# Performance work log

Hardware: AMD Instinct MI355X
Metric: run time of the kernel (lower is better)

## Reference

```python
import jax, jax.numpy as jnp
import numpy as np


def setup_inputs() -> dict:
    key = jax.random.key(0)
    ks = jax.random.split(key, 7)
    B, S, D_IN, D_K, D_V = 4, 4096, 1024, 64, 64
    s = 1.0 / np.sqrt(D_IN)
    return {
        "query": jax.random.normal(ks[0], (B, S, D_IN), jnp.float32),
        "key": jax.random.normal(ks[1], (B, S, D_IN), jnp.float32),
        "value": jax.random.normal(ks[2], (B, S, D_IN), jnp.float32),
        "Wq": jax.random.normal(ks[3], (D_IN, D_K), jnp.float32) * s,
        "bq": jnp.zeros((D_K,), jnp.float32),
        "Wk": jax.random.normal(ks[4], (D_IN, D_K), jnp.float32) * s,
        "bk": jnp.zeros((D_K,), jnp.float32),
        "Wv": jax.random.normal(ks[5], (D_IN, D_V), jnp.float32) * s,
        "bv": jnp.zeros((D_V,), jnp.float32),
    }


def reference(query, key, value, Wq, bq, Wk, bk, Wv, bv):
    # q(query) is computed twice in the original but is identical; compute once.
    q = query @ Wq + bq            # [B,S,dk]
    k = key @ Wk + bk              # [B,S,dk]
    v = value @ Wv + bv            # [B,S,dv]
    scale = jnp.asarray(q.shape[-1] ** 0.5, q.dtype)
    scores = jnp.einsum("bqd,bkd->bqk", q, k) / scale  # [B,S,S]
    probs = jax.nn.softmax(scores, axis=-1)
    return jnp.einsum("bqk,bkd->bqd", probs, v)        # [B,S,dv]
```

## Files before the change

kernel.cpp:

```cpp
#include <hip/hip_runtime.h>
#include <cmath>

constexpr int B_  = 4;
constexpr int S_  = 4096;
constexpr int DIN = 1024;
constexpr int DH  = 64;

typedef short bf16x8 __attribute__((ext_vector_type(8)));
typedef float f32x4  __attribute__((ext_vector_type(4)));

#define GPTR(p) (const __attribute__((address_space(1))) unsigned int*)(p)
#define LPTR(p) (__attribute__((address_space(3))) unsigned int*)(p)

__device__ __forceinline__ ushort f2bf(float x) {
    unsigned int u = __float_as_uint(x);
    return (ushort)((u + 0x7FFFu + ((u >> 16) & 1u)) >> 16);
}

__device__ __forceinline__ bf16x8 cvt8(float4 a, float4 b) {
    union { bf16x8 v; ushort u[8]; } r;
    r.u[0] = f2bf(a.x); r.u[1] = f2bf(a.y); r.u[2] = f2bf(a.z); r.u[3] = f2bf(a.w);
    r.u[4] = f2bf(b.x); r.u[5] = f2bf(b.y); r.u[6] = f2bf(b.z); r.u[7] = f2bf(b.w);
    return r.v;
}

#define QSCALE 0.18033688011112042f

__global__ __launch_bounds__(256) void setup_w(
    const float* __restrict__ Wq, const float* __restrict__ Wk,
    const float* __restrict__ Wv, ushort* __restrict__ Wt_g)
{
    const int y = blockIdx.y;
    const float* W = (y == 0) ? Wq : (y == 1) ? Wk : Wv;
    const int g    = blockIdx.x * 256 + threadIdx.x;
    const int lane = g & 63;
    const int nt   = (g >> 6) & 3;
    const int ks   = (g >> 8) & 1;
    const int it   = g >> 9;
    const int m    = lane & 15;
    const int quad = lane >> 4;
    const int n    = nt * 16 + m;
    const int k0   = it * 64 + (ks * 4 + quad) * 8;
    union { uint4 q; ushort u[8]; } r;
    #pragma unroll
    for (int i = 0; i < 8; ++i) r.u[i] = f2bf(W[(size_t)(k0 + i) * DH + n]);
    *(uint4*)(Wt_g + ((size_t)y << 16) + (size_t)g * 8) = r.q;
}

__global__ __launch_bounds__(256, 3) void proj_kernel(
    const float* __restrict__ Xq, const float* __restrict__ Xk, const float* __restrict__ Xv,
    const float* __restrict__ bq, const float* __restrict__ bk, const float* __restrict__ bv,
    const ushort* __restrict__ Wt_g,
    ushort* __restrict__ Qb, ushort* __restrict__ Kb, ushort* __restrict__ Vt)
{
    const int y = blockIdx.y;
    const float *X, *bias;
    if (y == 0)      { X = Xq; bias = bq; }
    else if (y == 1) { X = Xk; bias = bk; }
    else             { X = Xv; bias = bv; }

    __shared__ ushort Vx[64 * 72];

    const int tid  = threadIdx.x;
    const int w    = tid >> 6;
    const int lane = tid & 63;
    const int m    = lane & 15;
    const int quad = lane >> 4;
    const int row0 = blockIdx.x * 64;
    const int ph0  = (blockIdx.x + blockIdx.y * 5) & 15;

    const size_t  xrow = (size_t)(row0 + w * 16 + m) * DIN;
    const ushort* wsrc = Wt_g + ((size_t)y << 16) + (size_t)lane * 8;

    float bias_v[4];
    #pragma unroll
    for (int nt = 0; nt < 4; ++nt) bias_v[nt] = bias[nt * 16 + m];

    f32x4 acc[4] = {};
    float4 xb[2][4];
    uint4  wb[2][8];

    {
        const float* px = X + xrow + ph0 * 64 + quad * 8;
        xb[0][0] = *(const float4*)(px);      xb[0][1] = *(const float4*)(px + 4);
        xb[0][2] = *(const float4*)(px + 32); xb[0][3] = *(const float4*)(px + 36);
        #pragma unroll
        for (int f = 0; f < 8; ++f)
            wb[0][f] = *(const uint4*)(wsrc + (size_t)(ph0 * 8 + f) * 512);
    }

    #pragma unroll
    for (int it = 0; it < 16; ++it) {
        const int cb = it & 1, nb = cb ^ 1;
        if (it < 15) {
            const int wi = (it + 1 + ph0) & 15;
            const float* px = X + xrow + wi * 64 + quad * 8;
            xb[nb][0] = *(const float4*)(px);      xb[nb][1] = *(const float4*)(px + 4);
            xb[nb][2] = *(const float4*)(px + 32); xb[nb][3] = *(const float4*)(px + 36);
            #pragma unroll
            for (int f = 0; f < 8; ++f)
                wb[nb][f] = *(const uint4*)(wsrc + (size_t)(wi * 8 + f) * 512);
        }
        __builtin_amdgcn_sched_barrier(0);
        #pragma unroll
        for (int ks = 0; ks < 2; ++ks) {
            const bf16x8 a = cvt8(xb[cb][ks * 2], xb[cb][ks * 2 + 1]);
            #pragma unroll
            for (int nt = 0; nt < 4; ++nt)
                acc[nt] = __builtin_amdgcn_mfma_f32_16x16x32_bf16(
                    a, *(const bf16x8*)&wb[cb][ks * 4 + nt], acc[nt], 0, 0, 0);
        }
        __builtin_amdgcn_sched_barrier(0);
    }

    if (y < 2) {
        ushort* Out = (y == 0) ? Qb : Kb;
        const float sc = (y == 0) ? QSCALE : 1.0f;
        #pragma unroll
        for (int nt = 0; nt < 4; ++nt)
            #pragma unroll
            for (int j = 0; j < 4; ++j) {
                const int row = row0 + w * 16 + quad * 4 + j;
                Out[(size_t)row * DH + nt * 16 + m] = f2bf((acc[nt][j] + bias_v[nt]) * sc);
            }
    } else {
        #pragma unroll
        for (int nt = 0; nt < 4; ++nt)
            #pragma unroll
            for (int j = 0; j < 4; ++j) {
                const int d = nt * 16 + m;
                const int s = w * 16 + quad * 4 + j;
                Vx[d * 72 + (((s >> 3) ^ (d & 7)) * 8) + (s & 7)] = f2bf(acc[nt][j] + bias_v[nt]);
            }
        __syncthreads();
        const int batch = row0 >> 12;
        const int s0    = row0 & 4095;
        for (int i = tid; i < 512; i += 256) {
            const int d = i >> 3, c = i & 7;
            const uint4 v = *(const uint4*)&Vx[d * 72 + ((c ^ (d & 7)) * 8)];
            *(uint4*)(Vt + ((size_t)batch * 64 + d) * S_ + s0 + c * 8) = v;
        }
    }
}

__global__ __launch_bounds__(256, 4) void attn_kernel(
    const ushort* __restrict__ Qb, const ushort* __restrict__ Kb,
    const ushort* __restrict__ Vt, float* __restrict__ Opart, float* __restrict__ Lpart)
{
    __shared__ ushort Ks[64 * 64];
    __shared__ ushort Vs[64 * 64];
    __shared__ ushort Pt[64 * 72];

    const int tid  = threadIdx.x;
    const int w    = tid >> 6;
    const int lane = tid & 63;
    const int m    = lane & 15;
    const int quad = lane >> 4;
    const int b    = blockIdx.z, jc = blockIdx.y, qt = blockIdx.x;
    const int q0   = qt * 64;

    bf16x8 qf[2];
    #pragma unroll
    for (int ks = 0; ks < 2; ++ks)
        qf[ks] = *(const bf16x8*)(Qb + (size_t)(b * S_ + q0 + w * 16 + m) * 64
                                     + ks * 32 + quad * 8);

    f32x4 acc_o[4] = {};
    float Lp[4] = {};

    const ushort* kbase = Kb + (size_t)b * S_ * 64;
    const ushort* vbase = Vt + (size_t)b * 64 * S_;

    for (int it = 0; it < 16; ++it) {
        const int jt = jc * 16 + it;
        __syncthreads();
        #pragma unroll
        for (int i = 0; i < 2; ++i) {
            const int slot = w * 128 + i * 64 + lane;
            const int j = slot >> 3, c = slot & 7;
            __builtin_amdgcn_global_load_lds(
                GPTR(kbase + (size_t)(jt * 64 + j) * 64 + ((c ^ (j & 7)) * 8)),
                LPTR(&Ks[(w * 128 + i * 64) * 8]), 16, 0, 0);
            __builtin_amdgcn_global_load_lds(
                GPTR(vbase + (size_t)j * S_ + jt * 64 + ((c ^ (j & 7)) * 8)),
                LPTR(&Vs[(w * 128 + i * 64) * 8]), 16, 0, 0);
        }
        __syncthreads();

        f32x4 acc_s[4] = {};
        #pragma unroll
        for (int ks = 0; ks < 2; ++ks)
            #pragma unroll
            for (int jt4 = 0; jt4 < 4; ++jt4) {
                const int j = jt4 * 16 + m;
                const bf16x8 kf = *(const bf16x8*)&Ks[j * 64 + (((ks * 4 + quad) ^ (j & 7)) * 8)];
                acc_s[jt4] = __builtin_amdgcn_mfma_f32_16x16x32_bf16(
                    qf[ks], kf, acc_s[jt4], 0, 0, 0);
            }

        #pragma unroll
        for (int jt4 = 0; jt4 < 4; ++jt4)
            #pragma unroll
            for (int r = 0; r < 4; ++r) {
                const float e = exp2f(acc_s[jt4][r]);
                Lp[r] += e;
                Pt[(w * 16 + quad * 4 + r) * 72 + jt4 * 16 + m] = f2bf(e);
            }

        #pragma unroll
        for (int jc2 = 0; jc2 < 2; ++jc2) {
            const bf16x8 pf = *(const bf16x8*)&Pt[(w * 16 + m) * 72 + jc2 * 32 + quad * 8];
            #pragma unroll
            for (int dt = 0; dt < 4; ++dt) {
                const int d = dt * 16 + m;
                const bf16x8 vf = *(const bf16x8*)&Vs[d * 64 + (((jc2 * 4 + quad) ^ (d & 7)) * 8)];
                acc_o[dt] = __builtin_amdgcn_mfma_f32_16x16x32_bf16(pf, vf, acc_o[dt], 0, 0, 0);
            }
        }
    }

    #pragma unroll
    for (int r = 0; r < 4; ++r) {
        float s = Lp[r];
        #pragma unroll
        for (int off = 1; off < 16; off <<= 1)
            s += __shfl_xor(s, off, 64);
        Lp[r] = s;
    }

    const size_t bj = (size_t)(b * 4 + jc);
    float* Ob = Opart + (bj << 18);
    #pragma unroll
    for (int dt = 0; dt < 4; ++dt)
        #pragma unroll
        for (int r = 0; r < 4; ++r) {
            const int row = q0 + w * 16 + quad * 4 + r;
            Ob[(size_t)row * 64 + dt * 16 + m] = acc_o[dt][r];
        }
    if (m == 0) {
        #pragma unroll
        for (int r = 0; r < 4; ++r)
            Lpart[bj * 4096 + q0 + w * 16 + quad * 4 + r] = Lp[r];
    }
}

__global__ __launch_bounds__(256) void reduce_kernel(
    const float* __restrict__ Opart, const float* __restrict__ Lpart, float* __restrict__ out)
{
    const int g    = blockIdx.x * 256 + threadIdx.x;
    const int base = g << 2;
    const int b    = base >> 18;
    const int rem  = base & 0x3FFFF;
    const int q    = rem >> 6;
    float4 o = make_float4(0.f, 0.f, 0.f, 0.f);
    float  l = 0.f;
    #pragma unroll
    for (int jcc = 0; jcc < 4; ++jcc) {
        const float4 p = *(const float4*)(Opart + (((size_t)(b * 4 + jcc)) << 18) + rem);
        o.x += p.x; o.y += p.y; o.z += p.z; o.w += p.w;
        l += Lpart[(size_t)(b * 4 + jcc) * 4096 + q];
    }
    const float inv = 1.0f / l;
    o.x *= inv; o.y *= inv; o.z *= inv; o.w *= inv;
    *(float4*)(out + base) = o;
}

extern "C" void kernel_launch(void* const* d_in, const int* in_sizes, int n_in,
                              void* d_out, int out_size, void* d_ws, size_t ws_size,
                              hipStream_t stream)
{
    const float* query = (const float*)d_in[0];
    const float* key_  = (const float*)d_in[1];
    const float* value = (const float*)d_in[2];
    const float* Wq    = (const float*)d_in[3];
    const float* bq    = (const float*)d_in[4];
    const float* Wk    = (const float*)d_in[5];
    const float* bk    = (const float*)d_in[6];
    const float* Wv    = (const float*)d_in[7];
    const float* bv    = (const float*)d_in[8];
    float* out = (float*)d_out;

    char* ws = (char*)d_ws;
    ushort* Qb    = (ushort*)(ws);
    ushort* Kb    = (ushort*)(ws + (2  << 20));
    ushort* Vt    = (ushort*)(ws + (4  << 20));
    float*  Opart = (float*) (ws + (6  << 20));
    float*  Lpart = (float*) (ws + (22 << 20));
    ushort* Wt_g  = (ushort*)(ws + (6  << 20));

    setup_w<<<dim3(32, 3), 256, 0, stream>>>(Wq, Wk, Wv, Wt_g);
    proj_kernel<<<dim3(256, 3), 256, 0, stream>>>(
        query, key_, value, bq, bk, bv, Wt_g, Qb, Kb, Vt);
    attn_kernel<<<dim3(64, 4, 4), 256, 0, stream>>>(Qb, Kb, Vt, Opart, Lpart);
    reduce_kernel<<<dim3(1024), 256, 0, stream>>>(Opart, Lpart, out);
}
```

Before: 259.8 us.

## Stage projection inputs through LDS with async global_load_lds double buffering

The projection kernel now copies X and weight tiles into shared memory using direct global-to-LDS loads, double-buffered two iterations ahead. Before, each wave kept them in register buffers. X rows are XOR-swizzled to avoid bank conflicts and are read back from LDS for the bf16 conversion and MFMA. The aim is to cut register pressure, drop the 3-blocks occupancy bound, and get coalesced, asynchronous memory traffic. In exchange it adds two barriers per iteration and 48KB of LDS per block, which limits occupancy.

```diff
diff --git a/kernel.cpp b/kernel.cpp
--- a/kernel.cpp
+++ b/kernel.cpp
@@ -11,16 +11,18 @@
 
 #define GPTR(p) (const __attribute__((address_space(1))) unsigned int*)(p)
 #define LPTR(p) (__attribute__((address_space(3))) unsigned int*)(p)
+#define LDSF4(p) (*(const __attribute__((address_space(3))) f32x4*)(p))
+#define LDSB8(p) (*(const __attribute__((address_space(3))) bf16x8*)(p))
 
 __device__ __forceinline__ ushort f2bf(float x) {
     unsigned int u = __float_as_uint(x);
     return (ushort)((u + 0x7FFFu + ((u >> 16) & 1u)) >> 16);
 }
 
-__device__ __forceinline__ bf16x8 cvt8(float4 a, float4 b) {
+__device__ __forceinline__ bf16x8 cvt8(f32x4 a, f32x4 b) {
     union { bf16x8 v; ushort u[8]; } r;
-    r.u[0] = f2bf(a.x); r.u[1] = f2bf(a.y); r.u[2] = f2bf(a.z); r.u[3] = f2bf(a.w);
-    r.u[4] = f2bf(b.x); r.u[5] = f2bf(b.y); r.u[6] = f2bf(b.z); r.u[7] = f2bf(b.w);
+    r.u[0] = f2bf(a[0]); r.u[1] = f2bf(a[1]); r.u[2] = f2bf(a[2]); r.u[3] = f2bf(a[3]);
+    r.u[4] = f2bf(b[0]); r.u[5] = f2bf(b[1]); r.u[6] = f2bf(b[2]); r.u[7] = f2bf(b[3]);
     return r.v;
 }
 
@@ -47,19 +49,19 @@
     *(uint4*)(Wt_g + ((size_t)y << 16) + (size_t)g * 8) = r.q;
 }
 
-__global__ __launch_bounds__(256, 3) void proj_kernel(
+__global__ __launch_bounds__(256) void proj_kernel(
     const float* __restrict__ Xq, const float* __restrict__ Xk, const float* __restrict__ Xv,
     const float* __restrict__ bq, const float* __restrict__ bk, const float* __restrict__ bv,
     const ushort* __restrict__ Wt_g,
     ushort* __restrict__ Qb, ushort* __restrict__ Kb, ushort* __restrict__ Vt)
 {
+    __shared__ __align__(16) char smem[49152];
+
     const int y = blockIdx.y;
     const float *X, *bias;
     if (y == 0)      { X = Xq; bias = bq; }
     else if (y == 1) { X = Xk; bias = bk; }
     else             { X = Xv; bias = bv; }
-
-    __shared__ ushort Vx[64 * 72];
 
     const int tid  = threadIdx.x;
     const int w    = tid >> 6;
@@ -67,50 +69,77 @@
     const int m    = lane & 15;
     const int quad = lane >> 4;
     const int row0 = blockIdx.x * 64;
-    const int ph0  = (blockIdx.x + blockIdx.y * 5) & 15;
-
-    const size_t  xrow = (size_t)(row0 + w * 16 + m) * DIN;
-    const ushort* wsrc = Wt_g + ((size_t)y << 16) + (size_t)lane * 8;
 
     float bias_v[4];
     #pragma unroll
     for (int nt = 0; nt < 4; ++nt) bias_v[nt] = bias[nt * 16 + m];
+    asm volatile("s_waitcnt vmcnt(0)" ::: "memory");
+    __builtin_amdgcn_sched_barrier(0);
+
+    const char* xsrc = (const char*)X + (size_t)row0 * 4096;
+    const char* wsrc = (const char*)Wt_g + ((size_t)y << 17);
+
+    auto stage = [&](int wi, int buf) {
+        char* xdst = smem + buf * 16384;
+        char* wdst = smem + 32768 + buf * 8192;
+        #pragma unroll
+        for (int i = 0; i < 4; ++i) {
+            const int ci  = w * 4 + i;
+            const int row = ci * 4 + (lane >> 4);
+            const int ug  = (lane & 15) ^ (row & 7);
+            __builtin_amdgcn_global_load_lds(
+                GPTR(xsrc + (size_t)row * 4096 + wi * 256 + ug * 16),
+                LPTR(xdst + ci * 1024 + lane * 16), 16, 0, 0);
+        }
+        #pragma unroll
+        for (int i = 0; i < 2; ++i) {
+            const int f = w * 2 + i;
+            __builtin_amdgcn_global_load_lds(
+                GPTR(wsrc + (size_t)(wi * 8 + f) * 1024 + lane * 16),
+                LPTR(wdst + f * 1024 + lane * 16), 16, 0, 0);
+        }
+    };
+
+    stage(0, 0);
+    stage(1, 1);
 
     f32x4 acc[4] = {};
-    float4 xb[2][4];
-    uint4  wb[2][8];
-
-    {
-        const float* px = X + xrow + ph0 * 64 + quad * 8;
-        xb[0][0] = *(const float4*)(px);      xb[0][1] = *(const float4*)(px + 4);
-        xb[0][2] = *(const float4*)(px + 32); xb[0][3] = *(const float4*)(px + 36);
-        #pragma unroll
-        for (int f = 0; f < 8; ++f)
-            wb[0][f] = *(const uint4*)(wsrc + (size_t)(ph0 * 8 + f) * 512);
-    }
+    const int row = w * 16 + m;
 
     #pragma unroll
     for (int it = 0; it < 16; ++it) {
-        const int cb = it & 1, nb = cb ^ 1;
-        if (it < 15) {
-            const int wi = (it + 1 + ph0) & 15;
-            const float* px = X + xrow + wi * 64 + quad * 8;
-            xb[nb][0] = *(const float4*)(px);      xb[nb][1] = *(const float4*)(px + 4);
-            xb[nb][2] = *(const float4*)(px + 32); xb[nb][3] = *(const float4*)(px + 36);
-            #pragma unroll
-            for (int f = 0; f < 8; ++f)
-                wb[nb][f] = *(const uint4*)(wsrc + (size_t)(wi * 8 + f) * 512);
-        }
+        if (it < 15) asm volatile("s_waitcnt vmcnt(6)" ::: "memory");
+        else         asm volatile("s_waitcnt vmcnt(0)" ::: "memory");
         __builtin_amdgcn_sched_barrier(0);
+        __builtin_amdgcn_s_barrier();
+        __builtin_amdgcn_sched_barrier(0);
+
+        const char* xb = smem + (it & 1) * 16384;
+        const char* wb = smem + 32768 + (it & 1) * 8192;
+
+        f32x4 xv[4];
+        #pragma unroll
+        for (int ks = 0; ks < 2; ++ks)
+            #pragma unroll
+            for (int h = 0; h < 2; ++h) {
+                const int ug = ks * 8 + quad * 2 + h;
+                const int us = ug ^ (m & 7);
+                xv[ks * 2 + h] = LDSF4(xb + row * 256 + us * 16);
+            }
         #pragma unroll
         for (int ks = 0; ks < 2; ++ks) {
-            const bf16x8 a = cvt8(xb[cb][ks * 2], xb[cb][ks * 2 + 1]);
-            #pragma unroll
-            for (int nt = 0; nt < 4; ++nt)
-                acc[nt] = __builtin_amdgcn_mfma_f32_16x16x32_bf16(
-                    a, *(const bf16x8*)&wb[cb][ks * 4 + nt], acc[nt], 0, 0, 0);
-        }
+            const bf16x8 a = cvt8(xv[ks * 2], xv[ks * 2 + 1]);
+            #pragma unroll
+            for (int nt = 0; nt < 4; ++nt) {
+                const bf16x8 bfr = LDSB8(wb + (ks * 4 + nt) * 1024 + lane * 16);
+                acc[nt] = __builtin_amdgcn_mfma_f32_16x16x32_bf16(a, bfr, acc[nt], 0, 0, 0);
+            }
+        }
+
         __builtin_amdgcn_sched_barrier(0);
+        __builtin_amdgcn_s_barrier();
+        __builtin_amdgcn_sched_barrier(0);
+        if (it + 2 < 16) stage(it + 2, it & 1);
     }
 
     if (y < 2) {
@@ -120,10 +149,12 @@
         for (int nt = 0; nt < 4; ++nt)
             #pragma unroll
             for (int j = 0; j < 4; ++j) {
-                const int row = row0 + w * 16 + quad * 4 + j;
-                Out[(size_t)row * DH + nt * 16 + m] = f2bf((acc[nt][j] + bias_v[nt]) * sc);
+                const int r = row0 + w * 16 + quad * 4 + j;
+                Out[(size_t)r * DH + nt * 16 + m] = f2bf((acc[nt][j] + bias_v[nt]) * sc);
             }
     } else {
+        __syncthreads();
+        ushort* Vx = (ushort*)smem;
         #pragma unroll
         for (int nt = 0; nt < 4; ++nt)
             #pragma unroll
```

New measurement: 259.2 us. About the same (-0.2%).
